# Optimization experiments

Measured on AMD Instinct MI355X. Metric: run time of the kernel, lower is better.

## Reference

```python
import math
import jax, jax.numpy as jnp
import numpy as np

NH, NKV, HD, THETA = 32, 8, 128, 500000.0

def rotate_half(x):
    x1, x2 = jnp.split(x, 2, axis=-1)
    return jnp.concatenate((-x2, x1), axis=-1)

def rope_cos_sin(seq_len, dim, base, dtype):
    inv_freq = 1.0 / (base ** (jnp.arange(0, dim, 2, dtype=jnp.float32) / dim))
    t = jnp.arange(seq_len, dtype=jnp.float32)
    freqs = jnp.outer(t, inv_freq)              # [S, dim/2]
    emb = jnp.concatenate((freqs, freqs), -1)   # [S, dim]
    return jnp.cos(emb).astype(dtype), jnp.sin(emb).astype(dtype)

def setup_inputs() -> dict:
    key = jax.random.key(0)
    ks = jax.random.split(key, 5)
    B, S, H = 1, 2048, 4096
    sc = 1.0 / math.sqrt(H)
    return {
        'x':  jax.random.normal(ks[0], (B, S, H), jnp.float32),
        'wq': jax.random.normal(ks[1], (H, H), jnp.float32) * sc,
        'wk': jax.random.normal(ks[2], (NKV * HD, H), jnp.float32) * sc,
        'wv': jax.random.normal(ks[3], (NKV * HD, H), jnp.float32) * sc,
        'wo': jax.random.normal(ks[4], (H, H), jnp.float32) * sc,
    }

def attention(x, wq, wk, wv, wo):
    B, S, H = x.shape
    n_rep = NH // NKV
    q = (x @ wq.T).reshape(B, S, NH, HD).transpose(0, 2, 1, 3)    # [B,NH,S,HD]
    k = (x @ wk.T).reshape(B, S, NKV, HD).transpose(0, 2, 1, 3)   # [B,NKV,S,HD]
    v = (x @ wv.T).reshape(B, S, NKV, HD).transpose(0, 2, 1, 3)
    cos, sin = rope_cos_sin(S, HD, THETA, x.dtype)                # [S,HD]
    cos = cos[None, None]; sin = sin[None, None]
    q = q * cos + rotate_half(q) * sin
    k = k * cos + rotate_half(k) * sin
    k = jnp.repeat(k, n_rep, axis=1)                               # [B,NH,S,HD]
    v = jnp.repeat(v, n_rep, axis=1)
    scores = jnp.einsum('bhqd,bhkd->bhqk', q, k) / math.sqrt(HD)
    causal = jnp.tril(jnp.ones((S, S), dtype=bool))
    scores = jnp.where(causal, scores, jnp.finfo(scores.dtype).min)
    probs = jax.nn.softmax(scores, axis=-1)
    out = jnp.einsum('bhqk,bhkd->bhqd', probs, v)                  # [B,NH,S,HD]
    out = out.transpose(0, 2, 1, 3).reshape(B, S, H)
    return out @ wo.T

def reference(x, wq, wk, wv, wo):
    return attention(x, wq, wk, wv, wo)
```

## Files before the change

### kernel.cpp

```cpp
#include <hip/hip_runtime.h>
#include <hip/hip_bf16.h>
#include <math.h>

typedef __bf16 bf16x8 __attribute__((ext_vector_type(8)));
typedef __bf16 bf16x4 __attribute__((ext_vector_type(4)));
typedef unsigned short u16x8 __attribute__((ext_vector_type(8)));
typedef float  f32x4  __attribute__((ext_vector_type(4)));

constexpr int kS   = 2048;
constexpr int kH   = 4096;
constexpr int kNH  = 32;
constexpr int kNKV = 8;
constexpr int kHD  = 128;
constexpr int kQKV = kH + 2 * kNKV * kHD;
constexpr int kKOff = kH;
constexpr int kVOff = kH + kNKV * kHD;

__global__ void cast_all(const float* __restrict__ x, const float* __restrict__ wq,
                         const float* __restrict__ wk, const float* __restrict__ wv,
                         const float* __restrict__ wo,
                         __bf16* __restrict__ xb, __bf16* __restrict__ wqkv,
                         __bf16* __restrict__ wob) {
    int i = blockIdx.x * 256 + threadIdx.x;
    float4 f;
    __bf16* dst;
    int di;
    if (i < (1 << 21)) {
        f = ((const float4*)x)[i];
        dst = xb; di = i;
    } else {
        int j = i - (1 << 21);
        if (j < (6 << 20)) {
            const float4* s = (j < (1 << 22)) ? ((const float4*)wq + j)
                            : (j < (5 << 20)) ? ((const float4*)wk + (j - (1 << 22)))
                                              : ((const float4*)wv + (j - (5 << 20)));
            f = *s;
            dst = wqkv; di = j;
        } else {
            int k = j - (6 << 20);
            f = ((const float4*)wo)[k];
            dst = wob; di = k;
        }
    }
    bf16x4 o;
    o[0] = (__bf16)f.x; o[1] = (__bf16)f.y; o[2] = (__bf16)f.z; o[3] = (__bf16)f.w;
    ((bf16x4*)dst)[di] = o;
}

__device__ inline void gld16(const __bf16* g, __bf16* l) {
    __builtin_amdgcn_global_load_lds((const __attribute__((address_space(1))) void*)g,
                                     (__attribute__((address_space(3))) void*)l, 16, 0, 0);
}

constexpr int GBK = 32, GBM = 128;

template <typename OutT, int GBN>
__global__ __launch_bounds__(512, 2) void gemm8(const __bf16* __restrict__ A,
                                                const __bf16* __restrict__ B,
                                                OutT* __restrict__ C,
                                                int M, int N, int K, int nbx) {
    constexpr int FM  = 4;
    constexpr int FN  = GBN / 64;
    constexpr int AL  = GBM / 128;
    constexpr int BL  = GBN / 128;
    constexpr int GPK = AL + BL;
    constexpr int ASZ = GBM * GBK;
    constexpr int BSZ = GBN * GBK;

    __shared__ __align__(16) __bf16 Ab[4][ASZ];
    __shared__ __align__(16) __bf16 Bb[4][BSZ];

    const int tid = threadIdx.x, w = tid >> 6, lane = tid & 63;
    const int lr = lane & 15, g = lane >> 4;

    const int nwg = (int)gridDim.x;
    const int bid = (int)blockIdx.x;
    int trow, tcol;
    if (nwg == 256 && nbx == 16) {
        const int xcd = bid & 7, j = bid >> 3;
        trow = (xcd >> 1) * 4 + (j >> 3);
        tcol = (xcd & 1) * 8 + (j & 7);
    } else {
        const int id2 = (bid & 7) * (nwg >> 3) + (bid >> 3);
        trow = id2 / nbx; tcol = id2 % nbx;
    }
    const int m0 = trow * GBM, n0 = tcol * GBN;

    const int wm = (w >> 2) * 64, wn = (w & 3) * (GBN / 4);

    const __bf16* ga[AL]; int la[AL];
    const __bf16* gb[BL]; int lb[BL];
#pragma unroll
    for (int a = 0; a < AL; a++) {
        int G = a * 512 + tid, row = G >> 2;
        int lg = (G & 3) ^ ((row >> 1) & 3);
        ga[a] = A + (size_t)(m0 + row) * K + lg * 8;
        la[a] = G * 8;
    }
#pragma unroll
    for (int b = 0; b < BL; b++) {
        int G = b * 512 + tid, row = G >> 2;
        int lg = (G & 3) ^ ((row >> 1) & 3);
        gb[b] = B + (size_t)(n0 + row) * K + lg * 8;
        lb[b] = G * 8;
    }

    int pao[FM], pbo[FN];
    const int sw = (lr >> 1) & 3;
#pragma unroll
    for (int i = 0; i < FM; i++) pao[i] = (wm + i * 16 + lr) * GBK + ((g ^ sw) * 8);
#pragma unroll
    for (int j = 0; j < FN; j++) pbo[j] = (wn + j * 16 + lr) * GBK + ((g ^ sw) * 8);

    f32x4 acc[FM][FN];
#pragma unroll
    for (int i = 0; i < FM; i++)
#pragma unroll
        for (int j = 0; j < FN; j++) acc[i][j] = (f32x4)(0.f);

    const int NT = K / GBK;

#pragma unroll
    for (int z = 0; z < 3; z++) {
#pragma unroll
        for (int a = 0; a < AL; a++) gld16(ga[a] + z * GBK, &Ab[z][la[a]]);
#pragma unroll
        for (int b = 0; b < BL; b++) gld16(gb[b] + z * GBK, &Bb[z][lb[b]]);
    }
    if constexpr (GPK == 4) asm volatile("s_waitcnt vmcnt(8)" ::: "memory");
    else                    asm volatile("s_waitcnt vmcnt(6)" ::: "memory");
    __builtin_amdgcn_s_barrier();

    for (int Z = 0; Z < NT; ++Z) {
        const int q = Z & 3, qs = (Z + 3) & 3;

        bf16x8 af[FM], bfr[FN];
#pragma unroll
        for (int i = 0; i < FM; i++) af[i]  = *(const bf16x8*)&Ab[q][pao[i]];
#pragma unroll
        for (int j = 0; j < FN; j++) bfr[j] = *(const bf16x8*)&Bb[q][pbo[j]];

        if (Z < NT - 3) {
#pragma unroll
            for (int a = 0; a < AL; a++) gld16(ga[a] + (Z + 3) * GBK, &Ab[qs][la[a]]);
#pragma unroll
            for (int b = 0; b < BL; b++) gld16(gb[b] + (Z + 3) * GBK, &Bb[qs][lb[b]]);
        }

        __builtin_amdgcn_s_barrier();
        __builtin_amdgcn_s_setprio(1);
#pragma unroll
        for (int i = 0; i < FM; i++)
#pragma unroll
            for (int j = 0; j < FN; j++)
                acc[i][j] = __builtin_amdgcn_mfma_f32_16x16x32_bf16(
                    af[i], bfr[j], acc[i][j], 0, 0, 0);
        __builtin_amdgcn_s_setprio(0);

        if (Z < NT - 3) {
            if constexpr (GPK == 4) asm volatile("s_waitcnt vmcnt(8)" ::: "memory");
            else                    asm volatile("s_waitcnt vmcnt(6)" ::: "memory");
        } else if (Z == NT - 3) {
            if constexpr (GPK == 4) asm volatile("s_waitcnt vmcnt(4)" ::: "memory");
            else                    asm volatile("s_waitcnt vmcnt(3)" ::: "memory");
        } else if (Z == NT - 2) {
            asm volatile("s_waitcnt vmcnt(0)" ::: "memory");
        }
        __builtin_amdgcn_s_barrier();
    }

    const int cr = g * 4, cc = lr;
#pragma unroll
    for (int i = 0; i < FM; i++)
#pragma unroll
        for (int j = 0; j < FN; j++) {
            OutT* Cp = C + (size_t)(m0 + wm + i * 16 + cr) * N + (n0 + wn + j * 16 + cc);
#pragma unroll
            for (int r = 0; r < 4; r++) Cp[(size_t)r * N] = (OutT)acc[i][j][r];
        }
}

__global__ void rope_qkv(__bf16* __restrict__ qkv) {
    int idx  = blockIdx.x * 256 + threadIdx.x;
    int d8   = idx & 7;
    int rest = idx >> 3;
    int hh   = rest % (kNH + kNKV);
    int s    = rest / (kNH + kNKV);
    __bf16* base = qkv + (size_t)s * kQKV + ((hh < kNH) ? hh * kHD : kKOff + (hh - kNH) * kHD);
    float sc = (hh < kNH) ? 0.088388347648318447f : 1.0f;
    bf16x8 va = *(const bf16x8*)(base + d8 * 8);
    bf16x8 vb = *(const bf16x8*)(base + 64 + d8 * 8);
    bf16x8 ra, rb;
#pragma unroll
    for (int j = 0; j < 8; j++) {
        int d = d8 * 8 + j;
        float rev = (float)s * exp2f(fmaf((float)d, -0.2958057589f, -2.6514961295f));
        rev -= floorf(rev);
        float ang = rev * 6.28318530718f;
        float sn = __sinf(ang), cs = __cosf(ang);
        float a = (float)va[j], b = (float)vb[j];
        ra[j] = (__bf16)((a * cs - b * sn) * sc);
        rb[j] = (__bf16)((b * cs + a * sn) * sc);
    }
    *(bf16x8*)(base + d8 * 8)      = ra;
    *(bf16x8*)(base + 64 + d8 * 8) = rb;
}

constexpr int VTP = 72;

__global__ __launch_bounds__(256, 2) void flash_attn(const __bf16* __restrict__ qkv,
                                                     __bf16* __restrict__ ob) {
    __shared__ __align__(16) __bf16 Ks[64 * 128];
    __shared__ __align__(16) __bf16 Vt[128 * VTP];
    __shared__ __align__(16) __bf16 Ps[8 * 16 * 64];

    const int tid  = threadIdx.x;
    const int wave = tid >> 6, lane = tid & 63;
    const int bx   = blockIdx.x;
    const int kvh  = bx & 7;
    const int p    = bx >> 3;
    const int qt2  = (p < 32) ? (63 - p) : (p - 32);
    const int h    = kvh * 4 + wave;
    const int r    = lane & 15, g = lane >> 4;
    const int r7   = r & 7;

    const __bf16* kbase = qkv + kKOff + kvh * kHD;
    const __bf16* vbase = qkv + kVOff + kvh * kHD;

    int krow[4], kgc[4];
#pragma unroll
    for (int c = 0; c < 4; c++) {
        krow[c] = wave * 16 + c * 4 + (lane >> 4);
        kgc[c]  = (lane & 15) ^ (krow[c] & 15);
    }
    int vp[2], vc[2];
#pragma unroll
    for (int i = 0; i < 2; i++) {
        int task = i * 256 + tid;
        vp[i] = task & 31; vc[i] = task >> 5;
    }

    bf16x8 qfrag[2][4];
#pragma unroll
    for (int f = 0; f < 2; f++) {
        const __bf16* qrow = qkv + (size_t)(qt2 * 32 + f * 16 + r) * kQKV + h * kHD + g * 8;
#pragma unroll
        for (int c = 0; c < 4; c++) qfrag[f][c] = *(const bf16x8*)(qrow + c * 32);
    }

    f32x4 o[2][8];
#pragma unroll
    for (int f = 0; f < 2; f++)
#pragma unroll
        for (int dt = 0; dt < 8; dt++) o[f][dt] = (f32x4)(0.f);
    float mrow[2] = {-3.0e38f, -3.0e38f}, lrow[2] = {0.f, 0.f};

    const int nkt = qt2 / 2 + 1;
    for (int kt = 0; kt < nkt; ++kt) {
#pragma unroll
        for (int c = 0; c < 4; c++)
            gld16(kbase + (size_t)(kt * 64 + krow[c]) * kQKV + kgc[c] * 8,
                  Ks + (wave * 4 + c) * 512);
        bf16x8 va[2], vb[2];
#pragma unroll
        for (int i = 0; i < 2; i++) {
            const __bf16* v0 = vbase + (size_t)(kt * 64 + 2 * vp[i]) * kQKV + vc[i] * 8;
            va[i] = *(const bf16x8*)v0;
            vb[i] = *(const bf16x8*)(v0 + kQKV);
        }
        asm volatile("s_waitcnt vmcnt(0)" ::: "memory");
#pragma unroll
        for (int i = 0; i < 2; i++) {
            u16x8 a = __builtin_bit_cast(u16x8, va[i]);
            u16x8 b = __builtin_bit_cast(u16x8, vb[i]);
#pragma unroll
            for (int j = 0; j < 8; j++) {
                unsigned int pk = (unsigned int)a[j] | ((unsigned int)b[j] << 16);
                *(unsigned int*)(&Vt[(vc[i] * 8 + j) * VTP + 2 * vp[i]]) = pk;
            }
        }
        __syncthreads();

        f32x4 st[2][4];
#pragma unroll
        for (int f = 0; f < 2; f++)
#pragma unroll
            for (int t = 0; t < 4; t++) st[f][t] = (f32x4)(0.f);
        __builtin_amdgcn_s_setprio(1);
#pragma unroll
        for (int c = 0; c < 4; c++) {
#pragma unroll
            for (int t = 0; t < 4; t++) {
                bf16x8 kf = *(const bf16x8*)&Ks[(t * 16 + r) * 128 + (((c * 4 + g) ^ r) * 8)];
                st[0][t] = __builtin_amdgcn_mfma_f32_16x16x32_bf16(kf, qfrag[0][c], st[0][t], 0, 0, 0);
                st[1][t] = __builtin_amdgcn_mfma_f32_16x16x32_bf16(kf, qfrag[1][c], st[1][t], 0, 0, 0);
            }
        }
        __builtin_amdgcn_s_setprio(0);

        if (kt == nkt - 1) {
#pragma unroll
            for (int f = 0; f < 2; f++) {
                const int qg = qt2 * 32 + f * 16 + r;
#pragma unroll
                for (int t = 0; t < 4; t++)
#pragma unroll
                    for (int reg = 0; reg < 4; reg++) {
                        int key = kt * 64 + t * 16 + g * 4 + reg;
                        if (key > qg) st[f][t][reg] = -3.0e38f;
                    }
            }
        }

#pragma unroll
        for (int f = 0; f < 2; f++) {
            float mloc = -3.0e38f;
#pragma unroll
            for (int t = 0; t < 4; t++)
#pragma unroll
                for (int reg = 0; reg < 4; reg++) mloc = fmaxf(mloc, st[f][t][reg]);
            mloc = fmaxf(mloc, __shfl_xor(mloc, 16));
            mloc = fmaxf(mloc, __shfl_xor(mloc, 32));
            float mnew  = fmaxf(mrow[f], mloc);
            float alpha = __expf(mrow[f] - mnew);
            mrow[f] = mnew;
            float lsum = 0.f;
#pragma unroll
            for (int t = 0; t < 4; t++)
#pragma unroll
                for (int reg = 0; reg < 4; reg++) {
                    float pv = __expf(st[f][t][reg] - mnew);
                    st[f][t][reg] = pv;
                    lsum += pv;
                }
            lsum += __shfl_xor(lsum, 16);
            lsum += __shfl_xor(lsum, 32);
            lrow[f] = lrow[f] * alpha + lsum;

            float ar[4];
#pragma unroll
            for (int reg = 0; reg < 4; reg++) ar[reg] = __shfl(alpha, g * 4 + reg);
#pragma unroll
            for (int dt = 0; dt < 8; dt++)
#pragma unroll
                for (int reg = 0; reg < 4; reg++) o[f][dt][reg] *= ar[reg];

            __bf16* Pw = Ps + (wave * 2 + f) * 1024;
#pragma unroll
            for (int t = 0; t < 4; t++) {
                bf16x4 pb;
#pragma unroll
                for (int j = 0; j < 4; j++) pb[j] = (__bf16)st[f][t][j];
                int p8 = t * 4 + g;
                *(bf16x4*)&Pw[r * 64 + (((p8 >> 1) ^ r7) * 8) + ((p8 & 1) * 4)] = pb;
            }
        }
        __asm__ volatile("s_waitcnt lgkmcnt(0)" ::: "memory");

        __builtin_amdgcn_s_setprio(1);
#pragma unroll
        for (int kc = 0; kc < 2; kc++) {
            bf16x8 pf0 = *(const bf16x8*)&Ps[(wave * 2 + 0) * 1024 + r * 64 + (((kc * 4 + g) ^ r7) * 8)];
            bf16x8 pf1 = *(const bf16x8*)&Ps[(wave * 2 + 1) * 1024 + r * 64 + (((kc * 4 + g) ^ r7) * 8)];
#pragma unroll
            for (int dt = 0; dt < 8; dt++) {
                bf16x8 vf = *(const bf16x8*)&Vt[(dt * 16 + r) * VTP + kc * 32 + g * 8];
                o[0][dt] = __builtin_amdgcn_mfma_f32_16x16x32_bf16(pf0, vf, o[0][dt], 0, 0, 0);
                o[1][dt] = __builtin_amdgcn_mfma_f32_16x16x32_bf16(pf1, vf, o[1][dt], 0, 0, 0);
            }
        }
        __builtin_amdgcn_s_setprio(0);
        __syncthreads();
    }

#pragma unroll
    for (int f = 0; f < 2; f++) {
        float linv = 1.f / lrow[f];
        float lr4[4];
#pragma unroll
        for (int reg = 0; reg < 4; reg++) lr4[reg] = __shfl(linv, g * 4 + reg);
#pragma unroll
        for (int dt = 0; dt < 8; dt++)
#pragma unroll
            for (int reg = 0; reg < 4; reg++) {
                int qq = g * 4 + reg, dd = dt * 16 + r;
                ob[(size_t)(qt2 * 32 + f * 16 + qq) * kH + h * kHD + dd]
                    = (__bf16)(o[f][dt][reg] * lr4[reg]);
            }
    }
}

extern "C" void kernel_launch(void* const* d_in, const int* in_sizes, int n_in,
                              void* d_out, int out_size, void* d_ws, size_t ws_size,
                              hipStream_t stream) {
    const float* x  = (const float*)d_in[0];
    const float* wq = (const float*)d_in[1];
    const float* wk = (const float*)d_in[2];
    const float* wv = (const float*)d_in[3];
    const float* wo = (const float*)d_in[4];
    float* out = (float*)d_out;

    char* p = (char*)d_ws;
    auto alloc = [&](size_t bytes) {
        char* r = p;
        p += (bytes + 255) & ~(size_t)255;
        return r;
    };
    __bf16* xb    = (__bf16*)alloc((size_t)kS * kH * 2);
    __bf16* wqkvb = (__bf16*)alloc((size_t)kQKV * kH * 2);
    __bf16* qkv   = (__bf16*)alloc((size_t)kS * kQKV * 2);
    __bf16* wob   = (__bf16*)alloc((size_t)kH * kH * 2);
    __bf16* ao    = xb;

    cast_all<<<dim3(49152), 256, 0, stream>>>(x, wq, wk, wv, wo, xb, wqkvb, wob);

    gemm8<__bf16, 384><<<dim3((kS / GBM) * (kQKV / 384)), 512, 0, stream>>>(
        xb, wqkvb, qkv, kS, kQKV, kH, kQKV / 384);

    rope_qkv<<<dim3(kS * (kNH + kNKV) * 8 / 256), 256, 0, stream>>>(qkv);

    flash_attn<<<dim3(kNKV * (kS / 32)), 256, 0, stream>>>(qkv, ao);

    gemm8<float, 256><<<dim3((kS / GBM) * (kH / 256)), 512, 0, stream>>>(
        ao, wob, out, kS, kH, kH, kH / 256);
}
```

Baseline: 488.9 us.

## Double-buffer K tiles and prefetch V in flash attention; split wo cast

```diff
diff --git a/kernel.cpp b/kernel.cpp
--- a/kernel.cpp
+++ b/kernel.cpp
@@ -16,11 +16,19 @@
 constexpr int kKOff = kH;
 constexpr int kVOff = kH + kNKV * kHD;
 
+__global__ void cast_bf16(const float* __restrict__ in, __bf16* __restrict__ out, int n4) {
+    int i = blockIdx.x * blockDim.x + threadIdx.x;
+    if (i < n4) {
+        float4 f = ((const float4*)in)[i];
+        bf16x4 o;
+        o[0] = (__bf16)f.x; o[1] = (__bf16)f.y; o[2] = (__bf16)f.z; o[3] = (__bf16)f.w;
+        ((bf16x4*)out)[i] = o;
+    }
+}
+
 __global__ void cast_all(const float* __restrict__ x, const float* __restrict__ wq,
                          const float* __restrict__ wk, const float* __restrict__ wv,
-                         const float* __restrict__ wo,
-                         __bf16* __restrict__ xb, __bf16* __restrict__ wqkv,
-                         __bf16* __restrict__ wob) {
+                         __bf16* __restrict__ xb, __bf16* __restrict__ wqkv) {
     int i = blockIdx.x * 256 + threadIdx.x;
     float4 f;
     __bf16* dst;
@@ -30,17 +38,11 @@
         dst = xb; di = i;
     } else {
         int j = i - (1 << 21);
-        if (j < (6 << 20)) {
-            const float4* s = (j < (1 << 22)) ? ((const float4*)wq + j)
-                            : (j < (5 << 20)) ? ((const float4*)wk + (j - (1 << 22)))
-                                              : ((const float4*)wv + (j - (5 << 20)));
-            f = *s;
-            dst = wqkv; di = j;
-        } else {
-            int k = j - (6 << 20);
-            f = ((const float4*)wo)[k];
-            dst = wob; di = k;
-        }
+        const float4* s = (j < (1 << 22)) ? ((const float4*)wq + j)
+                        : (j < (5 << 20)) ? ((const float4*)wk + (j - (1 << 22)))
+                                          : ((const float4*)wv + (j - (5 << 20)));
+        f = *s;
+        dst = wqkv; di = j;
     }
     bf16x4 o;
     o[0] = (__bf16)f.x; o[1] = (__bf16)f.y; o[2] = (__bf16)f.z; o[3] = (__bf16)f.w;
@@ -210,7 +212,7 @@
 
 __global__ __launch_bounds__(256, 2) void flash_attn(const __bf16* __restrict__ qkv,
                                                      __bf16* __restrict__ ob) {
-    __shared__ __align__(16) __bf16 Ks[64 * 128];
+    __shared__ __align__(16) __bf16 Ks[2][64 * 128];
     __shared__ __align__(16) __bf16 Vt[128 * VTP];
     __shared__ __align__(16) __bf16 Ps[8 * 16 * 64];
 
@@ -256,30 +258,46 @@
     float mrow[2] = {-3.0e38f, -3.0e38f}, lrow[2] = {0.f, 0.f};
 
     const int nkt = qt2 / 2 + 1;
+
+    bf16x8 va[2], vb[2];
+#pragma unroll
+    for (int c = 0; c < 4; c++)
+        gld16(kbase + (size_t)krow[c] * kQKV + kgc[c] * 8, &Ks[0][(wave * 4 + c) * 512]);
+#pragma unroll
+    for (int i = 0; i < 2; i++) {
+        const __bf16* v0 = vbase + (size_t)(2 * vp[i]) * kQKV + vc[i] * 8;
+        va[i] = *(const bf16x8*)v0;
+        vb[i] = *(const bf16x8*)(v0 + kQKV);
+    }
+    asm volatile("s_waitcnt vmcnt(0)" ::: "memory");
+#pragma unroll
+    for (int i = 0; i < 2; i++) {
+        u16x8 a = __builtin_bit_cast(u16x8, va[i]);
+        u16x8 b = __builtin_bit_cast(u16x8, vb[i]);
+#pragma unroll
+        for (int j = 0; j < 8; j++) {
+            unsigned int pk = (unsigned int)a[j] | ((unsigned int)b[j] << 16);
+            *(unsigned int*)(&Vt[(vc[i] * 8 + j) * VTP + 2 * vp[i]]) = pk;
+        }
+    }
+    __syncthreads();
+
     for (int kt = 0; kt < nkt; ++kt) {
-#pragma unroll
-        for (int c = 0; c < 4; c++)
-            gld16(kbase + (size_t)(kt * 64 + krow[c]) * kQKV + kgc[c] * 8,
-                  Ks + (wave * 4 + c) * 512);
-        bf16x8 va[2], vb[2];
-#pragma unroll
-        for (int i = 0; i < 2; i++) {
-            const __bf16* v0 = vbase + (size_t)(kt * 64 + 2 * vp[i]) * kQKV + vc[i] * 8;
-            va[i] = *(const bf16x8*)v0;
-            vb[i] = *(const bf16x8*)(v0 + kQKV);
-        }
-        asm volatile("s_waitcnt vmcnt(0)" ::: "memory");
-#pragma unroll
-        for (int i = 0; i < 2; i++) {
-            u16x8 a = __builtin_bit_cast(u16x8, va[i]);
-            u16x8 b = __builtin_bit_cast(u16x8, vb[i]);
-#pragma unroll
-            for (int j = 0; j < 8; j++) {
-                unsigned int pk = (unsigned int)a[j] | ((unsigned int)b[j] << 16);
-                *(unsigned int*)(&Vt[(vc[i] * 8 + j) * VTP + 2 * vp[i]]) = pk;
-            }
-        }
-        __syncthreads();
+        const int cur = kt & 1, nb = cur ^ 1;
+        const bool nxt = (kt + 1) < nkt;
+
+        if (nxt) {
+#pragma unroll
+            for (int c = 0; c < 4; c++)
+                gld16(kbase + (size_t)((kt + 1) * 64 + krow[c]) * kQKV + kgc[c] * 8,
+                      &Ks[nb][(wave * 4 + c) * 512]);
+#pragma unroll
+            for (int i = 0; i < 2; i++) {
+                const __bf16* v0 = vbase + (size_t)((kt + 1) * 64 + 2 * vp[i]) * kQKV + vc[i] * 8;
+                va[i] = *(const bf16x8*)v0;
+                vb[i] = *(const bf16x8*)(v0 + kQKV);
+            }
+        }
 
         f32x4 st[2][4];
 #pragma unroll
@@ -291,7 +309,7 @@
         for (int c = 0; c < 4; c++) {
 #pragma unroll
             for (int t = 0; t < 4; t++) {
-                bf16x8 kf = *(const bf16x8*)&Ks[(t * 16 + r) * 128 + (((c * 4 + g) ^ r) * 8)];
+                bf16x8 kf = *(const bf16x8*)&Ks[cur][(t * 16 + r) * 128 + (((c * 4 + g) ^ r) * 8)];
                 st[0][t] = __builtin_amdgcn_mfma_f32_16x16x32_bf16(kf, qfrag[0][c], st[0][t], 0, 0, 0);
                 st[1][t] = __builtin_amdgcn_mfma_f32_16x16x32_bf16(kf, qfrag[1][c], st[1][t], 0, 0, 0);
             }
@@ -370,7 +388,22 @@
             }
         }
         __builtin_amdgcn_s_setprio(0);
-        __syncthreads();
+
+        if (nxt) {
+            __syncthreads();
+            asm volatile("s_waitcnt vmcnt(0)" ::: "memory");
+#pragma unroll
+            for (int i = 0; i < 2; i++) {
+                u16x8 a = __builtin_bit_cast(u16x8, va[i]);
+                u16x8 b = __builtin_bit_cast(u16x8, vb[i]);
+#pragma unroll
+                for (int j = 0; j < 8; j++) {
+                    unsigned int pk = (unsigned int)a[j] | ((unsigned int)b[j] << 16);
+                    *(unsigned int*)(&Vt[(vc[i] * 8 + j) * VTP + 2 * vp[i]]) = pk;
+                }
+            }
+            __syncthreads();
+        }
     }
 
 #pragma unroll
@@ -412,13 +445,15 @@
     __bf16* wob   = (__bf16*)alloc((size_t)kH * kH * 2);
     __bf16* ao    = xb;
 
-    cast_all<<<dim3(49152), 256, 0, stream>>>(x, wq, wk, wv, wo, xb, wqkvb, wob);
+    cast_all<<<dim3(1 << 15), 256, 0, stream>>>(x, wq, wk, wv, xb, wqkvb);
 
     gemm8<__bf16, 384><<<dim3((kS / GBM) * (kQKV / 384)), 512, 0, stream>>>(
         xb, wqkvb, qkv, kS, kQKV, kH, kQKV / 384);
 
     rope_qkv<<<dim3(kS * (kNH + kNKV) * 8 / 256), 256, 0, stream>>>(qkv);
 
+    cast_bf16<<<dim3((kH * kH / 4) / 256), 256, 0, stream>>>(wo, wob, kH * kH / 4);
+
     flash_attn<<<dim3(kNKV * (kS / 32)), 256, 0, stream>>>(qkv, ao);
 
     gemm8<float, 256><<<dim3((kS / GBM) * (kH / 256)), 512, 0, stream>>>(
```

Measured after the change: 474.8 us. 1.03x faster.
